# Kernel optimization log

Measured on AMD Instinct MI355X. Metric: run time of the kernel, lower is better.

The kernel has to match this reference:

```python
import jax, jax.numpy as jnp
import numpy as np

N, D_IN, H0, H1, K = 32768, 3000, 1024, 256, 20
V = 1.0  # Student-t degrees of freedom (self.v)


def setup_inputs() -> dict:
    key = jax.random.key(0)
    ks = jax.random.split(key, 6)
    # Xavier-ish scales for linear layers (torch Linear default is uniform; scale only affects stats)
    x = jax.random.normal(ks[0], (N, D_IN), dtype=jnp.float32)
    W1 = jax.random.normal(ks[1], (D_IN, H0), dtype=jnp.float32) * (1.0 / np.sqrt(D_IN))
    b1 = jnp.zeros((H0,), dtype=jnp.float32)
    W2 = jax.random.normal(ks[2], (H0, H1), dtype=jnp.float32) * (1.0 / np.sqrt(H0))
    b2 = jnp.zeros((H1,), dtype=jnp.float32)
    # xavier_normal_ for cluster_layer: std = sqrt(2/(K+H1))
    clusters = jax.random.normal(ks[3], (K, H1), dtype=jnp.float32) * np.sqrt(2.0 / (K + H1))
    return {"x": x, "W1": W1, "b1": b1, "W2": W2, "b2": b2, "clusters": clusters}


def reference(x, W1, b1, W2, b2, clusters):
    # fc: Linear -> SiLU -> Linear
    h = jax.nn.silu(x @ W1 + b1)          # [N, H0]
    z = h @ W2 + b2                        # [N, H1]
    # soft_assign: Student-t kernel over squared distances to cluster centroids
    d2 = jnp.sum((z[:, None, :] - clusters[None, :, :]) ** 2, axis=2)  # [N, K]
    q = 1.0 / (1.0 + d2 / V)
    q = q ** ((V + 1.0) / 2.0)
    q = q / jnp.sum(q, axis=1, keepdims=True)  # row-normalize
    return z, q
```

## Files before the change

kernel.cpp:

```cpp
#include <hip/hip_runtime.h>
#include <stdint.h>
#include <stddef.h>

#define N_ROWS 32768
#define D_IN   3000
#define KPAD   3072
#define H0     1024
#define H1     256
#define NCLUST 20

typedef __attribute__((ext_vector_type(8))) short short8;
typedef __attribute__((ext_vector_type(4))) float f32x4;

__device__ inline unsigned short f2bf(float f) {
    union { float f; unsigned u; } v; v.f = f;
    unsigned r = v.u + 0x7fffu + ((v.u >> 16) & 1u);
    return (unsigned short)(r >> 16);
}

__device__ inline void async16(const unsigned short* g, unsigned short* l) {
    __builtin_amdgcn_global_load_lds(
        (const __attribute__((address_space(1))) unsigned int*)(g),
        (__attribute__((address_space(3))) unsigned int*)(l),
        16, 0, 0);
}

__global__ __launch_bounds__(256)
void cvt_x(const float* __restrict__ x, unsigned short* __restrict__ xb) {
    int idx = blockIdx.x * 256 + threadIdx.x;
    int m  = idx / 768;
    int k4 = idx - m * 768;
    if (m >= N_ROWS) return;
    uint2 out;
    if (k4 < 750) {
        const float4 v = ((const float4*)x)[(size_t)m * 750 + k4];
        out.x = ((unsigned)f2bf(v.x)) | (((unsigned)f2bf(v.y)) << 16);
        out.y = ((unsigned)f2bf(v.z)) | (((unsigned)f2bf(v.w)) << 16);
    } else {
        out.x = 0u; out.y = 0u;
    }
    ((uint2*)xb)[(size_t)m * 768 + k4] = out;
}

__global__ __launch_bounds__(256)
void transpose_cvt(const float* __restrict__ W, int rows, int cols, int rowsPad,
                   unsigned short* __restrict__ outT) {
    __shared__ unsigned short tile[32][33];
    const int c0 = blockIdx.x * 32;
    const int r0 = blockIdx.y * 32;
    const int tx = threadIdx.x, ty = threadIdx.y;
    #pragma unroll
    for (int i = 0; i < 4; ++i) {
        int r = r0 + ty + i * 8;
        float v = (r < rows) ? W[(size_t)r * cols + c0 + tx] : 0.0f;
        tile[ty + i * 8][tx] = f2bf(v);
    }
    __syncthreads();
    #pragma unroll
    for (int i = 0; i < 4; ++i) {
        int c = c0 + ty + i * 8;
        outT[(size_t)c * rowsPad + r0 + tx] = tile[tx][ty + i * 8];
    }
}

template<int EPILOGUE>
__global__ __launch_bounds__(256)
void gemm_tn(const unsigned short* __restrict__ A,
             const unsigned short* __restrict__ Bt,
             const float* __restrict__ bias,
             void* __restrict__ Cout, int Nn, int K)
{
    __shared__ unsigned short sA[128 * 32];
    __shared__ unsigned short sB[128 * 32];

    const int m0   = blockIdx.y * 128;
    const int n0   = blockIdx.x * 128;
    const int tid  = threadIdx.x;
    const int wave = tid >> 6;
    const int lane = tid & 63;
    const int wm   = wave & 1;
    const int wn   = wave >> 1;

    f32x4 acc[4][4];
    #pragma unroll
    for (int i = 0; i < 4; ++i)
        #pragma unroll
        for (int j = 0; j < 4; ++j)
            acc[i][j] = (f32x4){0.f, 0.f, 0.f, 0.f};

    const int sRow0 = wave * 32 + (lane >> 2);
    const int sCol  = (lane & 3) * 8;
    const unsigned short* gA0 = A  + (size_t)(m0 + sRow0) * K + sCol;
    const unsigned short* gA1 = gA0 + (size_t)16 * K;
    const unsigned short* gB0 = Bt + (size_t)(n0 + sRow0) * K + sCol;
    const unsigned short* gB1 = gB0 + (size_t)16 * K;
    unsigned short* lA0 = &sA[wave * 1024];
    unsigned short* lA1 = lA0 + 512;
    unsigned short* lB0 = &sB[wave * 1024];
    unsigned short* lB1 = lB0 + 512;

    const int fa = (wm * 64 + (lane & 15)) * 32 + (lane >> 4) * 8;
    const int fb = (wn * 64 + (lane & 15)) * 32 + (lane >> 4) * 8;

    for (int k0 = 0; k0 < K; k0 += 32) {
        async16(gA0 + k0, lA0);
        async16(gA1 + k0, lA1);
        async16(gB0 + k0, lB0);
        async16(gB1 + k0, lB1);
        __syncthreads();

        short8 af[4], bf[4];
        #pragma unroll
        for (int t = 0; t < 4; ++t) {
            af[t] = *(const short8*)&sA[fa + t * 16 * 32];
            bf[t] = *(const short8*)&sB[fb + t * 16 * 32];
        }
        #pragma unroll
        for (int i = 0; i < 4; ++i)
            #pragma unroll
            for (int j = 0; j < 4; ++j)
                acc[i][j] = __builtin_amdgcn_mfma_f32_16x16x32_bf16(
                    af[i], bf[j], acc[i][j], 0, 0, 0);
        __syncthreads();
    }

    const int cr = (lane >> 4) * 4;
    const int cc = lane & 15;
    #pragma unroll
    for (int j = 0; j < 4; ++j) {
        const int col = n0 + wn * 64 + j * 16 + cc;
        const float bv = bias[col];
        #pragma unroll
        for (int i = 0; i < 4; ++i) {
            const int rowBase = m0 + wm * 64 + i * 16 + cr;
            #pragma unroll
            for (int r = 0; r < 4; ++r) {
                float v = acc[i][j][r] + bv;
                if (EPILOGUE == 0) {
                    float s = v / (1.0f + __expf(-v));
                    ((unsigned short*)Cout)[(size_t)(rowBase + r) * Nn + col] = f2bf(s);
                } else {
                    ((float*)Cout)[(size_t)(rowBase + r) * Nn + col] = v;
                }
            }
        }
    }
}

__global__ __launch_bounds__(256)
void cluster_kernel(const float* __restrict__ z, const float* __restrict__ clusters,
                    float* __restrict__ q) {
    __shared__ float sc[NCLUST * H1];
    const int tid = threadIdx.x;
    for (int i = tid; i < NCLUST * H1; i += 256) sc[i] = clusters[i];
    __syncthreads();

    const int wave = tid >> 6, lane = tid & 63;
    const int row = blockIdx.x * 4 + wave;

    const float4 zv = ((const float4*)(z + (size_t)row * H1))[lane];

    float myq = 0.0f, qsum = 0.0f;
    #pragma unroll
    for (int k = 0; k < NCLUST; ++k) {
        const float4 cv = ((const float4*)(sc + k * H1))[lane];
        float dx = zv.x - cv.x, dy = zv.y - cv.y;
        float dz = zv.z - cv.z, dw = zv.w - cv.w;
        float p = dx * dx + dy * dy + dz * dz + dw * dw;
        #pragma unroll
        for (int s = 32; s >= 1; s >>= 1) p += __shfl_xor(p, s, 64);
        float qk = 1.0f / (1.0f + p);
        qsum += qk;
        myq = (lane == k) ? qk : myq;
    }
    if (lane < NCLUST) q[(size_t)row * NCLUST + lane] = myq / qsum;
}

extern "C" void kernel_launch(void* const* d_in, const int* in_sizes, int n_in,
                              void* d_out, int out_size, void* d_ws, size_t ws_size,
                              hipStream_t stream) {
    const float* x        = (const float*)d_in[0];
    const float* W1       = (const float*)d_in[1];
    const float* b1       = (const float*)d_in[2];
    const float* W2       = (const float*)d_in[3];
    const float* b2       = (const float*)d_in[4];
    const float* clusters = (const float*)d_in[5];
    float* out = (float*)d_out;

    unsigned short* xb  = (unsigned short*)d_ws;
    unsigned short* w1t = xb  + (size_t)N_ROWS * KPAD;
    unsigned short* w2t = w1t + (size_t)H0 * KPAD;
    unsigned short* h   = w2t + (size_t)H1 * H0;

    hipLaunchKernelGGL(cvt_x, dim3((N_ROWS * 768) / 256), dim3(256), 0, stream, x, xb);
    hipLaunchKernelGGL(transpose_cvt, dim3(H0 / 32, KPAD / 32), dim3(32, 8), 0, stream,
                       W1, D_IN, H0, KPAD, w1t);
    hipLaunchKernelGGL(transpose_cvt, dim3(H1 / 32, H0 / 32), dim3(32, 8), 0, stream,
                       W2, H0, H1, H0, w2t);
    hipLaunchKernelGGL((gemm_tn<0>), dim3(H0 / 128, N_ROWS / 128), dim3(256), 0, stream,
                       xb, w1t, b1, (void*)h, H0, KPAD);
    hipLaunchKernelGGL((gemm_tn<1>), dim3(H1 / 128, N_ROWS / 128), dim3(256), 0, stream,
                       h, w2t, b2, (void*)out, H1, H0);
    hipLaunchKernelGGL(cluster_kernel, dim3(N_ROWS / 4), dim3(256), 0, stream,
                       out, clusters, out + (size_t)N_ROWS * H1);
}
```

Baseline: 991.0 us.

## Double-buffer GEMM LDS tiles, widen N tile to 256, vectorize x conversion

```diff
diff --git a/kernel.cpp b/kernel.cpp
--- a/kernel.cpp
+++ b/kernel.cpp
@@ -28,18 +28,20 @@
 __global__ __launch_bounds__(256)
 void cvt_x(const float* __restrict__ x, unsigned short* __restrict__ xb) {
     int idx = blockIdx.x * 256 + threadIdx.x;
-    int m  = idx / 768;
-    int k4 = idx - m * 768;
-    if (m >= N_ROWS) return;
-    uint2 out;
-    if (k4 < 750) {
-        const float4 v = ((const float4*)x)[(size_t)m * 750 + k4];
-        out.x = ((unsigned)f2bf(v.x)) | (((unsigned)f2bf(v.y)) << 16);
-        out.y = ((unsigned)f2bf(v.z)) | (((unsigned)f2bf(v.w)) << 16);
+    int m  = idx / 384;
+    int k8 = idx - m * 384;
+    uint4 out;
+    if (k8 < 375) {
+        const float4 v0 = ((const float4*)x)[(size_t)m * 750 + k8 * 2];
+        const float4 v1 = ((const float4*)x)[(size_t)m * 750 + k8 * 2 + 1];
+        out.x = ((unsigned)f2bf(v0.x)) | (((unsigned)f2bf(v0.y)) << 16);
+        out.y = ((unsigned)f2bf(v0.z)) | (((unsigned)f2bf(v0.w)) << 16);
+        out.z = ((unsigned)f2bf(v1.x)) | (((unsigned)f2bf(v1.y)) << 16);
+        out.w = ((unsigned)f2bf(v1.z)) | (((unsigned)f2bf(v1.w)) << 16);
     } else {
-        out.x = 0u; out.y = 0u;
-    }
-    ((uint2*)xb)[(size_t)m * 768 + k4] = out;
+        out.x = 0u; out.y = 0u; out.z = 0u; out.w = 0u;
+    }
+    ((uint4*)xb)[(size_t)m * 384 + k8] = out;
 }
 
 __global__ __launch_bounds__(256)
@@ -64,71 +66,86 @@
 }
 
 template<int EPILOGUE>
-__global__ __launch_bounds__(256)
+__global__ __launch_bounds__(256, 2)
 void gemm_tn(const unsigned short* __restrict__ A,
              const unsigned short* __restrict__ Bt,
              const float* __restrict__ bias,
              void* __restrict__ Cout, int Nn, int K)
 {
-    __shared__ unsigned short sA[128 * 32];
-    __shared__ unsigned short sB[128 * 32];
+    __shared__ unsigned short sA[2][128 * 32];
+    __shared__ unsigned short sB[2][256 * 32];
 
     const int m0   = blockIdx.y * 128;
-    const int n0   = blockIdx.x * 128;
+    const int n0   = blockIdx.x * 256;
     const int tid  = threadIdx.x;
     const int wave = tid >> 6;
     const int lane = tid & 63;
     const int wm   = wave & 1;
     const int wn   = wave >> 1;
 
-    f32x4 acc[4][4];
+    f32x4 acc[4][8];
     #pragma unroll
     for (int i = 0; i < 4; ++i)
         #pragma unroll
-        for (int j = 0; j < 4; ++j)
+        for (int j = 0; j < 8; ++j)
             acc[i][j] = (f32x4){0.f, 0.f, 0.f, 0.f};
 
-    const int sRow0 = wave * 32 + (lane >> 2);
-    const int sCol  = (lane & 3) * 8;
-    const unsigned short* gA0 = A  + (size_t)(m0 + sRow0) * K + sCol;
+    const int laneRow = lane >> 2;
+    const int laneCol = (lane & 3) * 8;
+    const unsigned short* gA0 = A  + (size_t)(m0 + wave * 32 + laneRow) * K + laneCol;
     const unsigned short* gA1 = gA0 + (size_t)16 * K;
-    const unsigned short* gB0 = Bt + (size_t)(n0 + sRow0) * K + sCol;
+    const unsigned short* gB0 = Bt + (size_t)(n0 + wave * 64 + laneRow) * K + laneCol;
     const unsigned short* gB1 = gB0 + (size_t)16 * K;
-    unsigned short* lA0 = &sA[wave * 1024];
-    unsigned short* lA1 = lA0 + 512;
-    unsigned short* lB0 = &sB[wave * 1024];
-    unsigned short* lB1 = lB0 + 512;
-
-    const int fa = (wm * 64 + (lane & 15)) * 32 + (lane >> 4) * 8;
-    const int fb = (wn * 64 + (lane & 15)) * 32 + (lane >> 4) * 8;
-
-    for (int k0 = 0; k0 < K; k0 += 32) {
-        async16(gA0 + k0, lA0);
-        async16(gA1 + k0, lA1);
-        async16(gB0 + k0, lB0);
-        async16(gB1 + k0, lB1);
+    const unsigned short* gB2 = gB0 + (size_t)32 * K;
+    const unsigned short* gB3 = gB0 + (size_t)48 * K;
+    const int lAo = wave * 1024;
+    const int lBo = wave * 2048;
+
+    const int fa = (wm * 64  + (lane & 15)) * 32 + (lane >> 4) * 8;
+    const int fb = (wn * 128 + (lane & 15)) * 32 + (lane >> 4) * 8;
+
+    const int KT = K >> 5;
+
+    {
+        async16(gA0, &sA[0][lAo]);
+        async16(gA1, &sA[0][lAo + 512]);
+        async16(gB0, &sB[0][lBo]);
+        async16(gB1, &sB[0][lBo + 512]);
+        async16(gB2, &sB[0][lBo + 1024]);
+        async16(gB3, &sB[0][lBo + 1536]);
+    }
+
+    for (int kt = 0; kt < KT; ++kt) {
+        const int buf = kt & 1;
         __syncthreads();
-
-        short8 af[4], bf[4];
-        #pragma unroll
-        for (int t = 0; t < 4; ++t) {
-            af[t] = *(const short8*)&sA[fa + t * 16 * 32];
-            bf[t] = *(const short8*)&sB[fb + t * 16 * 32];
+        if (kt + 1 < KT) {
+            const int k0 = (kt + 1) << 5;
+            const int nb = buf ^ 1;
+            async16(gA0 + k0, &sA[nb][lAo]);
+            async16(gA1 + k0, &sA[nb][lAo + 512]);
+            async16(gB0 + k0, &sB[nb][lBo]);
+            async16(gB1 + k0, &sB[nb][lBo + 512]);
+            async16(gB2 + k0, &sB[nb][lBo + 1024]);
+            async16(gB3 + k0, &sB[nb][lBo + 1536]);
         }
+        short8 af[4], bf[8];
+        #pragma unroll
+        for (int t = 0; t < 4; ++t) af[t] = *(const short8*)&sA[buf][fa + t * 512];
+        #pragma unroll
+        for (int t = 0; t < 8; ++t) bf[t] = *(const short8*)&sB[buf][fb + t * 512];
         #pragma unroll
         for (int i = 0; i < 4; ++i)
             #pragma unroll
-            for (int j = 0; j < 4; ++j)
+            for (int j = 0; j < 8; ++j)
                 acc[i][j] = __builtin_amdgcn_mfma_f32_16x16x32_bf16(
                     af[i], bf[j], acc[i][j], 0, 0, 0);
-        __syncthreads();
     }
 
     const int cr = (lane >> 4) * 4;
     const int cc = lane & 15;
     #pragma unroll
-    for (int j = 0; j < 4; ++j) {
-        const int col = n0 + wn * 64 + j * 16 + cc;
+    for (int j = 0; j < 8; ++j) {
+        const int col = n0 + wn * 128 + j * 16 + cc;
         const float bv = bias[col];
         #pragma unroll
         for (int i = 0; i < 4; ++i) {
@@ -192,14 +209,14 @@
     unsigned short* w2t = w1t + (size_t)H0 * KPAD;
     unsigned short* h   = w2t + (size_t)H1 * H0;
 
-    hipLaunchKernelGGL(cvt_x, dim3((N_ROWS * 768) / 256), dim3(256), 0, stream, x, xb);
+    hipLaunchKernelGGL(cvt_x, dim3((N_ROWS * 384) / 256), dim3(256), 0, stream, x, xb);
     hipLaunchKernelGGL(transpose_cvt, dim3(H0 / 32, KPAD / 32), dim3(32, 8), 0, stream,
                        W1, D_IN, H0, KPAD, w1t);
     hipLaunchKernelGGL(transpose_cvt, dim3(H1 / 32, H0 / 32), dim3(32, 8), 0, stream,
                        W2, H0, H1, H0, w2t);
-    hipLaunchKernelGGL((gemm_tn<0>), dim3(H0 / 128, N_ROWS / 128), dim3(256), 0, stream,
+    hipLaunchKernelGGL((gemm_tn<0>), dim3(H0 / 256, N_ROWS / 128), dim3(256), 0, stream,
                        xb, w1t, b1, (void*)h, H0, KPAD);
-    hipLaunchKernelGGL((gemm_tn<1>), dim3(H1 / 128, N_ROWS / 128), dim3(256), 0, stream,
+    hipLaunchKernelGGL((gemm_tn<1>), dim3(H1 / 256, N_ROWS / 128), dim3(256), 0, stream,
                        h, w2t, b2, (void*)out, H1, H0);
     hipLaunchKernelGGL(cluster_kernel, dim3(N_ROWS / 4), dim3(256), 0, stream,
                        out, clusters, out + (size_t)N_ROWS * H1);
```

Result: faster. 894.9 us (-9.7%).
